# Performance work log

Measured on AMD Instinct MI355X. Metric: run time of the kernel, lower is better.

Reference implementation:

```python
import jax, jax.numpy as jnp
import numpy as np

B, S, D_MODEL, H_DIM = 8, 4096, 512, 120  # h = 1, so d_k = h_dim = 120
NEG_INF = jnp.float32(-1e9)
L2_EPS = 1e-12  # F.normalize eps


def setup_inputs() -> dict:
    key = jax.random.key(0)
    k_q, k_m, k_w, k_wt = jax.random.split(key, 4)
    query = jax.random.normal(k_q, (B, S, D_MODEL), dtype=jnp.float32)
    mask = jax.random.randint(k_m, (B, S, S), 0, 2, dtype=jnp.int32)
    # q_linear params (kaiming-uniform-ish init scale)
    lim = 1.0 / np.sqrt(D_MODEL)
    w_q = jax.random.uniform(k_w, (H_DIM, D_MODEL), jnp.float32, -lim, lim)
    b_q = jnp.zeros((H_DIM,), jnp.float32)
    # weight_tensor: shape (h, d_k) = (1, 120), xavier-uniform scale
    wt_lim = np.sqrt(6.0 / (1 + H_DIM))
    weight_tensor = jax.random.uniform(k_wt, (1, H_DIM), jnp.float32, -wt_lim, wt_lim)
    return {"query": query, "mask": mask, "w_q": w_q, "b_q": b_q,
            "weight_tensor": weight_tensor}


def reference(query, mask, w_q, b_q, weight_tensor):
    # context = q_linear(query).view(B, -1, h_dim); with h=1 the view is identity
    context = jnp.einsum("bsd,kd->bsk", query, w_q) + b_q          # [B, S, 120]
    # weighted then L2-normalized (cosine-similarity) features
    ctx = context * weight_tensor[:, None, :]                        # bcast (1,1,120)
    norm = jnp.sqrt(jnp.sum(ctx * ctx, axis=-1, keepdims=True))
    ctx_n = ctx / jnp.maximum(norm, L2_EPS)
    scores = jnp.einsum("bqk,bpk->bqp", ctx_n, ctx_n)               # [B, S, S]
    scores = jnp.where(mask == 0, NEG_INF, scores)                   # masked_fill
    return jax.nn.softmax(scores, axis=-1)                           # dropout: eval/identity
```

## Files before the change

kernel.cpp:

```cpp
#include <hip/hip_runtime.h>
#include <hip/hip_bf16.h>
#include <stdint.h>

#define BATCH 8
#define SEQ   4096
#define DM    512
#define HD    120
#define KP    128

typedef __bf16   v8bf  __attribute__((ext_vector_type(8)));
typedef float    v4f   __attribute__((ext_vector_type(4)));
typedef uint32_t u32x4 __attribute__((ext_vector_type(4)));
typedef uint32_t u32x2 __attribute__((ext_vector_type(2)));
typedef float    f32x4 __attribute__((ext_vector_type(4)));

static __device__ __forceinline__ ushort f2bf(float x) {
  uint32_t u = __builtin_bit_cast(uint32_t, x);
  return (ushort)((u + 0x7fffu + ((u >> 16) & 1u)) >> 16);
}

static __device__ __forceinline__ void gld16(const void* g, void* l) {
  __builtin_amdgcn_global_load_lds(
      (const __attribute__((address_space(1))) uint32_t*)g,
      (__attribute__((address_space(3))) uint32_t*)l, 16, 0, 0);
}

template <int NC>
static __device__ __forceinline__ void stage(const char* gsrc, char* lbase, int w, int lane) {
  #pragma unroll
  for (int i = 0; i < NC; ++i)
    gld16(gsrc + (w * NC + i) * 1024 + lane * 16, lbase + (w * NC + i) * 1024);
}

__global__ __launch_bounds__(256) void ctx_kernel(
    const float* __restrict__ q, const float* __restrict__ wq,
    const float* __restrict__ bq, const float* __restrict__ wt,
    ushort* __restrict__ ctx)
{
  __shared__ __align__(16) float qs[32][68];
  __shared__ __align__(16) float ws2[32][136];

  const int t  = threadIdx.x;
  const int tx = t & 31, ty = t >> 5;
  const size_t row0 = (size_t)blockIdx.x * 64;
  const int qr = t >> 2, qk = (t & 3) * 8;

  float acc[8][4];
  #pragma unroll
  for (int j = 0; j < 8; ++j)
    #pragma unroll
    for (int i = 0; i < 4; ++i) acc[j][i] = 0.f;

  for (int k0 = 0; k0 < DM; k0 += 32) {
    __syncthreads();
    {
      f32x4 v0 = *(const f32x4*)&q[(row0 + qr) * DM + k0 + qk];
      f32x4 v1 = *(const f32x4*)&q[(row0 + qr) * DM + k0 + qk + 4];
      #pragma unroll
      for (int i = 0; i < 4; ++i) qs[qk + i][qr] = v0[i];
      #pragma unroll
      for (int i = 0; i < 4; ++i) qs[qk + 4 + i][qr] = v1[i];
    }
    #pragma unroll
    for (int i = 0; i < 16; ++i) {
      int flat = t + i * 256;
      int kk = flat & 31, c = flat >> 5;
      ws2[kk][c] = (c < HD) ? wq[c * DM + k0 + kk] : 0.f;
    }
    __syncthreads();
    #pragma unroll
    for (int kk = 0; kk < 32; ++kk) {
      f32x4 b  = *(const f32x4*)&ws2[kk][tx * 4];
      f32x4 a0 = *(const f32x4*)&qs[kk][ty * 8];
      f32x4 a1 = *(const f32x4*)&qs[kk][ty * 8 + 4];
      #pragma unroll
      for (int r = 0; r < 4; ++r)
        #pragma unroll
        for (int c = 0; c < 4; ++c) {
          acc[r][c]     = fmaf(a0[r], b[c], acc[r][c]);
          acc[4 + r][c] = fmaf(a1[r], b[c], acc[4 + r][c]);
        }
    }
  }

  float wtv[4], bqv[4];
  #pragma unroll
  for (int i = 0; i < 4; ++i) {
    int c = tx * 4 + i;
    wtv[i] = (c < HD) ? wt[c] : 0.f;
    bqv[i] = (c < HD) ? bq[c] : 0.f;
  }
  #pragma unroll
  for (int j = 0; j < 8; ++j) {
    int r = ty * 8 + j;
    float v[4]; float ss = 0.f;
    #pragma unroll
    for (int i = 0; i < 4; ++i) {
      v[i] = (acc[j][i] + bqv[i]) * wtv[i];
      ss = fmaf(v[i], v[i], ss);
    }
    #pragma unroll
    for (int xm = 1; xm < 32; xm <<= 1) ss += __shfl_xor(ss, xm, 64);
    float rinv = 1.f / fmaxf(sqrtf(ss), 1e-12f);
    uint32_t p0 = (uint32_t)f2bf(v[0] * rinv) | ((uint32_t)f2bf(v[1] * rinv) << 16);
    uint32_t p1 = (uint32_t)f2bf(v[2] * rinv) | ((uint32_t)f2bf(v[3] * rinv) << 16);
    u32x2 o = {p0, p1};
    char* dst = (char*)ctx + (row0 + r) * 256 +
                (((tx >> 1) * 16) ^ ((r & 7) << 4)) + (tx & 1) * 8;
    *(u32x2*)dst = o;
  }
}

static __device__ __forceinline__ v8bf ldfrag(const char* base, int row, int kb) {
  int byte = row * 256 + (kb ^ ((row & 7) << 4));
  return __builtin_bit_cast(v8bf, *(const u32x4*)(base + byte));
}

#define DO_MFMA(BUF, ACC)                                                        \
  _Pragma("unroll")                                                              \
  for (int kk = 0; kk < 4; ++kk) {                                               \
    int kb = kk * 64 + g * 16;                                                   \
    v8bf a0 = ldfrag(A_s, wr * 32 + ln, kb);                                     \
    v8bf a1 = ldfrag(A_s, wr * 32 + 16 + ln, kb);                                \
    v8bf b0 = ldfrag(BUF, wc * 32 + ln, kb);                                     \
    v8bf b1 = ldfrag(BUF, wc * 32 + 16 + ln, kb);                                \
    ACC[0][0] = __builtin_amdgcn_mfma_f32_16x16x32_bf16(a0, b0, ACC[0][0], 0, 0, 0); \
    ACC[0][1] = __builtin_amdgcn_mfma_f32_16x16x32_bf16(a0, b1, ACC[0][1], 0, 0, 0); \
    ACC[1][0] = __builtin_amdgcn_mfma_f32_16x16x32_bf16(a1, b0, ACC[1][0], 0, 0, 0); \
    ACC[1][1] = __builtin_amdgcn_mfma_f32_16x16x32_bf16(a1, b1, ACC[1][1], 0, 0, 0); \
  }

#define LOADM(dst, jj)                                                           \
  do {                                                                           \
    int joff = (jj) * 128;                                                       \
    _Pragma("unroll") for (int rs = 0; rs < 2; ++rs)                             \
    _Pragma("unroll") for (int i2 = 0; i2 < 4; ++i2)                             \
    _Pragma("unroll") for (int cs = 0; cs < 2; ++cs)                             \
      dst[rs * 8 + cs * 4 + i2] = mrow[rs][i2][joff + cs * 16];                  \
  } while (0)

__global__ __launch_bounds__(512) void attn_kernel(
    const ushort* __restrict__ ctx, const int* __restrict__ mask,
    uint32_t* __restrict__ wsbits, float* __restrict__ out)
{
  __shared__ __align__(16) char lds[81920];
  char* A_s = lds;
  char* B0  = lds + 16384;
  char* B1  = lds + 49152;
  float* lW   = (float*)B1;
  float* lfin = (float*)(B1 + 1024);

  const int t    = threadIdx.x;
  const int b    = blockIdx.x & 7;
  const int tile = blockIdx.x >> 3;
  const int r0   = tile * 64;
  const int w    = t >> 6, lane = t & 63;
  const int wr   = w >> 2, wc = w & 3;
  const int g    = lane >> 4, ln = lane & 15;
  const char* ctxb = (const char*)ctx + (size_t)b * SEQ * 256;
  uint32_t* wsb = wsbits + (size_t)blockIdx.x * (512 * 16);
  const size_t mbase = ((size_t)b << 24) + ((size_t)r0 << 12);

  const int* mrow[2][4];
  #pragma unroll
  for (int rs = 0; rs < 2; ++rs)
    #pragma unroll
    for (int i = 0; i < 4; ++i) {
      int qrr = wr * 32 + rs * 16 + g * 4 + i;
      mrow[rs][i] = mask + mbase + ((size_t)qrr << 12) + wc * 32 + ln;
    }

  stage<2>(ctxb + (size_t)r0 * 256, A_s, w, lane);
  stage<4>(ctxb, B0, w, lane);
  int mcur[16];
  LOADM(mcur, 0);
  __syncthreads();

  float lpart[2][4];
  #pragma unroll
  for (int rs = 0; rs < 2; ++rs)
    #pragma unroll
    for (int i = 0; i < 4; ++i) lpart[rs][i] = 0.f;
  uint32_t curbits = 0;

  for (int j = 0; j < 32; ++j) {
    char* cur = (j & 1) ? B1 : B0;
    char* nxt = (j & 1) ? B0 : B1;
    if (j < 31) stage<4>(ctxb + (size_t)((j + 1) * 128) * 256, nxt, w, lane);
    int mnext[16];
    if (j < 31) LOADM(mnext, j + 1);

    v4f acc[2][2];
    #pragma unroll
    for (int rs = 0; rs < 2; ++rs)
      #pragma unroll
      for (int cs = 0; cs < 2; ++cs) acc[rs][cs] = (v4f){0.f, 0.f, 0.f, 0.f};
    DO_MFMA(cur, acc);

    uint32_t tb = 0;
    #pragma unroll
    for (int rs = 0; rs < 2; ++rs)
      #pragma unroll
      for (int cs = 0; cs < 2; ++cs)
        #pragma unroll
        for (int i = 0; i < 4; ++i) {
          int mk = mcur[rs * 8 + cs * 4 + i];
          float e = mk ? __expf(acc[rs][cs][i] - 1.0f) : 0.0f;
          lpart[rs][i] += e;
          tb |= (uint32_t)(mk != 0) << (rs * 8 + cs * 4 + i);
        }
    if (j & 1) wsb[(j >> 1) * 512 + t] = curbits | (tb << 16);
    else       curbits = tb;
    if (j < 31) {
      #pragma unroll
      for (int x = 0; x < 16; ++x) mcur[x] = mnext[x];
    }
    __syncthreads();
  }

  #pragma unroll
  for (int rs = 0; rs < 2; ++rs)
    #pragma unroll
    for (int i = 0; i < 4; ++i) {
      float s = lpart[rs][i];
      #pragma unroll
      for (int xm = 1; xm < 16; xm <<= 1) s += __shfl_xor(s, xm, 64);
      lpart[rs][i] = s;
    }
  if (ln == 0) {
    #pragma unroll
    for (int rs = 0; rs < 2; ++rs)
      #pragma unroll
      for (int i = 0; i < 4; ++i)
        lW[wc * 64 + wr * 32 + rs * 16 + g * 4 + i] = lpart[rs][i];
  }
  __syncthreads();
  if (t < 64) {
    float lf = lW[t] + lW[64 + t] + lW[128 + t] + lW[192 + t];
    lfin[t] = (lf > 0.f) ? (1.f / lf) : 0.f;
  }
  __syncthreads();
  float lir[2][4];
  #pragma unroll
  for (int rs = 0; rs < 2; ++rs)
    #pragma unroll
    for (int i = 0; i < 4; ++i)
      lir[rs][i] = lfin[wr * 32 + rs * 16 + g * 4 + i];

  stage<4>(ctxb, B0, w, lane);
  uint32_t bcur = wsb[t];
  uint32_t bnext = 0;
  __syncthreads();

  for (int j = 0; j < 32; ++j) {
    char* cur = (j & 1) ? B1 : B0;
    char* nxt = (j & 1) ? B0 : B1;
    if (j < 31) stage<4>(ctxb + (size_t)((j + 1) * 128) * 256, nxt, w, lane);
    if (!(j & 1) && j < 30) bnext = wsb[((j >> 1) + 1) * 512 + t];

    v4f acc[2][2];
    #pragma unroll
    for (int rs = 0; rs < 2; ++rs)
      #pragma unroll
      for (int cs = 0; cs < 2; ++cs) acc[rs][cs] = (v4f){0.f, 0.f, 0.f, 0.f};
    DO_MFMA(cur, acc);

    uint32_t bits = bcur >> ((j & 1) * 16);
    #pragma unroll
    for (int rs = 0; rs < 2; ++rs)
      #pragma unroll
      for (int cs = 0; cs < 2; ++cs)
        #pragma unroll
        for (int i = 0; i < 4; ++i) {
          int qrr = wr * 32 + rs * 16 + g * 4 + i;
          size_t off = mbase + ((size_t)qrr << 12) + j * 128 + wc * 32 + cs * 16 + ln;
          float val = ((bits >> (rs * 8 + cs * 4 + i)) & 1u)
                        ? __expf(acc[rs][cs][i] - 1.0f) * lir[rs][i] : 0.0f;
          __builtin_nontemporal_store(val, out + off);
        }
    if (j & 1) bcur = bnext;
    __syncthreads();
  }
}

extern "C" void kernel_launch(void* const* d_in, const int* in_sizes, int n_in,
                              void* d_out, int out_size, void* d_ws, size_t ws_size,
                              hipStream_t stream) {
  const float* query = (const float*)d_in[0];
  const int*   mask  = (const int*)d_in[1];
  const float* w_q   = (const float*)d_in[2];
  const float* b_q   = (const float*)d_in[3];
  const float* wt    = (const float*)d_in[4];
  float* out = (float*)d_out;

  ushort* ctx = (ushort*)d_ws;
  uint32_t* wsbits = (uint32_t*)((char*)d_ws +
      (size_t)BATCH * SEQ * KP * sizeof(ushort));

  ctx_kernel<<<dim3(BATCH * SEQ / 64), dim3(256), 0, stream>>>(query, w_q, b_q, wt, ctx);
  attn_kernel<<<dim3(BATCH * SEQ / 64), dim3(512), 0, stream>>>(ctx, mask, wsbits, out);
}
```

Before: 356.4 us.

## Restructure attention kernel to per-wave row strips with register-resident Q and direct global loads

Replaces the LDS-staged, block-tiled two-pass attention kernel with one where each wave owns 16 query rows, keeps its Q fragments in registers, and streams key fragments straight from global memory into registers with software double buffering. This removes LDS staging and the __syncthreads barriers. Mask and output accesses become 16-byte vector loads and stores along rows, and the ctx layout drops its XOR swizzle. The grid shrinks to 512 blocks of 256 threads, so occupancy falls, and key data is re-read from global or L2 by every wave instead of being shared through LDS.

```diff
diff --git a/kernel.cpp b/kernel.cpp
--- a/kernel.cpp
+++ b/kernel.cpp
@@ -6,30 +6,16 @@
 #define SEQ   4096
 #define DM    512
 #define HD    120
-#define KP    128
 
 typedef __bf16   v8bf  __attribute__((ext_vector_type(8)));
 typedef float    v4f   __attribute__((ext_vector_type(4)));
-typedef uint32_t u32x4 __attribute__((ext_vector_type(4)));
+typedef int      i4    __attribute__((ext_vector_type(4)));
 typedef uint32_t u32x2 __attribute__((ext_vector_type(2)));
 typedef float    f32x4 __attribute__((ext_vector_type(4)));
 
 static __device__ __forceinline__ ushort f2bf(float x) {
   uint32_t u = __builtin_bit_cast(uint32_t, x);
   return (ushort)((u + 0x7fffu + ((u >> 16) & 1u)) >> 16);
-}
-
-static __device__ __forceinline__ void gld16(const void* g, void* l) {
-  __builtin_amdgcn_global_load_lds(
-      (const __attribute__((address_space(1))) uint32_t*)g,
-      (__attribute__((address_space(3))) uint32_t*)l, 16, 0, 0);
-}
-
-template <int NC>
-static __device__ __forceinline__ void stage(const char* gsrc, char* lbase, int w, int lane) {
-  #pragma unroll
-  for (int i = 0; i < NC; ++i)
-    gld16(gsrc + (w * NC + i) * 1024 + lane * 16, lbase + (w * NC + i) * 1024);
 }
 
 __global__ __launch_bounds__(256) void ctx_kernel(
@@ -70,15 +56,15 @@
     __syncthreads();
     #pragma unroll
     for (int kk = 0; kk < 32; ++kk) {
-      f32x4 b  = *(const f32x4*)&ws2[kk][tx * 4];
+      f32x4 bv = *(const f32x4*)&ws2[kk][tx * 4];
       f32x4 a0 = *(const f32x4*)&qs[kk][ty * 8];
       f32x4 a1 = *(const f32x4*)&qs[kk][ty * 8 + 4];
       #pragma unroll
       for (int r = 0; r < 4; ++r)
         #pragma unroll
         for (int c = 0; c < 4; ++c) {
-          acc[r][c]     = fmaf(a0[r], b[c], acc[r][c]);
-          acc[4 + r][c] = fmaf(a1[r], b[c], acc[4 + r][c]);
+          acc[r][c]     = fmaf(a0[r], bv[c], acc[r][c]);
+          acc[4 + r][c] = fmaf(a1[r], bv[c], acc[4 + r][c]);
         }
     }
   }
@@ -105,181 +91,118 @@
     uint32_t p0 = (uint32_t)f2bf(v[0] * rinv) | ((uint32_t)f2bf(v[1] * rinv) << 16);
     uint32_t p1 = (uint32_t)f2bf(v[2] * rinv) | ((uint32_t)f2bf(v[3] * rinv) << 16);
     u32x2 o = {p0, p1};
-    char* dst = (char*)ctx + (row0 + r) * 256 +
-                (((tx >> 1) * 16) ^ ((r & 7) << 4)) + (tx & 1) * 8;
-    *(u32x2*)dst = o;
-  }
-}
-
-static __device__ __forceinline__ v8bf ldfrag(const char* base, int row, int kb) {
-  int byte = row * 256 + (kb ^ ((row & 7) << 4));
-  return __builtin_bit_cast(v8bf, *(const u32x4*)(base + byte));
-}
-
-#define DO_MFMA(BUF, ACC)                                                        \
-  _Pragma("unroll")                                                              \
-  for (int kk = 0; kk < 4; ++kk) {                                               \
-    int kb = kk * 64 + g * 16;                                                   \
-    v8bf a0 = ldfrag(A_s, wr * 32 + ln, kb);                                     \
-    v8bf a1 = ldfrag(A_s, wr * 32 + 16 + ln, kb);                                \
-    v8bf b0 = ldfrag(BUF, wc * 32 + ln, kb);                                     \
-    v8bf b1 = ldfrag(BUF, wc * 32 + 16 + ln, kb);                                \
-    ACC[0][0] = __builtin_amdgcn_mfma_f32_16x16x32_bf16(a0, b0, ACC[0][0], 0, 0, 0); \
-    ACC[0][1] = __builtin_amdgcn_mfma_f32_16x16x32_bf16(a0, b1, ACC[0][1], 0, 0, 0); \
-    ACC[1][0] = __builtin_amdgcn_mfma_f32_16x16x32_bf16(a1, b0, ACC[1][0], 0, 0, 0); \
-    ACC[1][1] = __builtin_amdgcn_mfma_f32_16x16x32_bf16(a1, b1, ACC[1][1], 0, 0, 0); \
-  }
-
-#define LOADM(dst, jj)                                                           \
-  do {                                                                           \
-    int joff = (jj) * 128;                                                       \
-    _Pragma("unroll") for (int rs = 0; rs < 2; ++rs)                             \
-    _Pragma("unroll") for (int i2 = 0; i2 < 4; ++i2)                             \
-    _Pragma("unroll") for (int cs = 0; cs < 2; ++cs)                             \
-      dst[rs * 8 + cs * 4 + i2] = mrow[rs][i2][joff + cs * 16];                  \
-  } while (0)
-
-__global__ __launch_bounds__(512) void attn_kernel(
+    *(u32x2*)((char*)ctx + (row0 + r) * 256 + tx * 8) = o;
+  }
+}
+
+#define MFMA(A, B, C) __builtin_amdgcn_mfma_f32_16x16x32_bf16(A, B, C, 0, 0, 0)
+
+#define LDP(dst, jc) do {                                                     \
+  const char* _p = ctxb + (size_t)((jc) * 32 + ln) * 256 + g * 16;            \
+  dst[0] = *(const v8bf*)(_p);         dst[1] = *(const v8bf*)(_p + 64);      \
+  dst[2] = *(const v8bf*)(_p + 128);   dst[3] = *(const v8bf*)(_p + 192);     \
+  dst[4] = *(const v8bf*)(_p + 4096);  dst[5] = *(const v8bf*)(_p + 4160);    \
+  dst[6] = *(const v8bf*)(_p + 4224);  dst[7] = *(const v8bf*)(_p + 4288);    \
+} while (0)
+
+#define LDM(dst, jc) do {                                                     \
+  dst[0] = *(const i4*)(mrow + (jc) * 32 + g * 4);                            \
+  dst[1] = *(const i4*)(mrow + (jc) * 32 + 16 + g * 4);                       \
+} while (0)
+
+#define QKT(pf, a0, a1) do {                                                  \
+  a0 = (v4f){0.f, 0.f, 0.f, 0.f}; a1 = (v4f){0.f, 0.f, 0.f, 0.f};             \
+  a0 = MFMA(pf[0], qf0, a0);  a1 = MFMA(pf[4], qf0, a1);                      \
+  a0 = MFMA(pf[1], qf1, a0);  a1 = MFMA(pf[5], qf1, a1);                      \
+  a0 = MFMA(pf[2], qf2, a0);  a1 = MFMA(pf[6], qf2, a1);                      \
+  a0 = MFMA(pf[3], qf3, a0);  a1 = MFMA(pf[7], qf3, a1);                      \
+} while (0)
+
+#define STEPA(pf, mf, jc, SH) do {                                            \
+  v4f a0, a1; QKT(pf, a0, a1);                                                \
+  uint32_t tb = 0;                                                            \
+  _Pragma("unroll")                                                           \
+  for (int i = 0; i < 4; ++i) {                                               \
+    float e0 = __expf(a0[i] - 1.f), e1 = __expf(a1[i] - 1.f);                 \
+    lsum += (mf[0][i] ? e0 : 0.f) + (mf[1][i] ? e1 : 0.f);                    \
+    tb |= (uint32_t)(mf[0][i] != 0) << i;                                     \
+    tb |= (uint32_t)(mf[1][i] != 0) << (4 + i);                               \
+  }                                                                           \
+  ubits |= tb << (SH);                                                        \
+  if ((SH) == 24) { wsb[((jc) >> 2) * 64 + lane] = ubits; ubits = 0; }        \
+} while (0)
+
+#define STEPB(pf, jc, SH) do {                                                \
+  v4f a0, a1; QKT(pf, a0, a1);                                                \
+  uint32_t bb = bcur >> (SH);                                                 \
+  f32x4 o0, o1;                                                               \
+  _Pragma("unroll")                                                           \
+  for (int i = 0; i < 4; ++i) {                                               \
+    o0[i] = ((bb >> i) & 1u)       ? __expf(a0[i] - 1.f) * lir : 0.f;         \
+    o1[i] = ((bb >> (4 + i)) & 1u) ? __expf(a1[i] - 1.f) * lir : 0.f;         \
+  }                                                                           \
+  *(f32x4*)(orow + (size_t)(jc) * 32 + g * 4) = o0;                           \
+  *(f32x4*)(orow + (size_t)(jc) * 32 + 16 + g * 4) = o1;                      \
+} while (0)
+
+__global__ __launch_bounds__(256) void attn_kernel(
     const ushort* __restrict__ ctx, const int* __restrict__ mask,
     uint32_t* __restrict__ wsbits, float* __restrict__ out)
 {
-  __shared__ __align__(16) char lds[81920];
-  char* A_s = lds;
-  char* B0  = lds + 16384;
-  char* B1  = lds + 49152;
-  float* lW   = (float*)B1;
-  float* lfin = (float*)(B1 + 1024);
-
   const int t    = threadIdx.x;
   const int b    = blockIdx.x & 7;
-  const int tile = blockIdx.x >> 3;
-  const int r0   = tile * 64;
   const int w    = t >> 6, lane = t & 63;
-  const int wr   = w >> 2, wc = w & 3;
-  const int g    = lane >> 4, ln = lane & 15;
+  const int ln   = lane & 15, g = lane >> 4;
+  const int qg   = (blockIdx.x >> 3) * 4 + w;
+  const int qrow = qg * 16 + ln;
   const char* ctxb = (const char*)ctx + (size_t)b * SEQ * 256;
-  uint32_t* wsb = wsbits + (size_t)blockIdx.x * (512 * 16);
-  const size_t mbase = ((size_t)b << 24) + ((size_t)r0 << 12);
-
-  const int* mrow[2][4];
-  #pragma unroll
-  for (int rs = 0; rs < 2; ++rs)
-    #pragma unroll
-    for (int i = 0; i < 4; ++i) {
-      int qrr = wr * 32 + rs * 16 + g * 4 + i;
-      mrow[rs][i] = mask + mbase + ((size_t)qrr << 12) + wc * 32 + ln;
-    }
-
-  stage<2>(ctxb + (size_t)r0 * 256, A_s, w, lane);
-  stage<4>(ctxb, B0, w, lane);
-  int mcur[16];
-  LOADM(mcur, 0);
-  __syncthreads();
-
-  float lpart[2][4];
-  #pragma unroll
-  for (int rs = 0; rs < 2; ++rs)
-    #pragma unroll
-    for (int i = 0; i < 4; ++i) lpart[rs][i] = 0.f;
-  uint32_t curbits = 0;
-
-  for (int j = 0; j < 32; ++j) {
-    char* cur = (j & 1) ? B1 : B0;
-    char* nxt = (j & 1) ? B0 : B1;
-    if (j < 31) stage<4>(ctxb + (size_t)((j + 1) * 128) * 256, nxt, w, lane);
-    int mnext[16];
-    if (j < 31) LOADM(mnext, j + 1);
-
-    v4f acc[2][2];
-    #pragma unroll
-    for (int rs = 0; rs < 2; ++rs)
-      #pragma unroll
-      for (int cs = 0; cs < 2; ++cs) acc[rs][cs] = (v4f){0.f, 0.f, 0.f, 0.f};
-    DO_MFMA(cur, acc);
-
-    uint32_t tb = 0;
-    #pragma unroll
-    for (int rs = 0; rs < 2; ++rs)
-      #pragma unroll
-      for (int cs = 0; cs < 2; ++cs)
-        #pragma unroll
-        for (int i = 0; i < 4; ++i) {
-          int mk = mcur[rs * 8 + cs * 4 + i];
-          float e = mk ? __expf(acc[rs][cs][i] - 1.0f) : 0.0f;
-          lpart[rs][i] += e;
-          tb |= (uint32_t)(mk != 0) << (rs * 8 + cs * 4 + i);
-        }
-    if (j & 1) wsb[(j >> 1) * 512 + t] = curbits | (tb << 16);
-    else       curbits = tb;
-    if (j < 31) {
-      #pragma unroll
-      for (int x = 0; x < 16; ++x) mcur[x] = mnext[x];
-    }
-    __syncthreads();
-  }
-
-  #pragma unroll
-  for (int rs = 0; rs < 2; ++rs)
-    #pragma unroll
-    for (int i = 0; i < 4; ++i) {
-      float s = lpart[rs][i];
-      #pragma unroll
-      for (int xm = 1; xm < 16; xm <<= 1) s += __shfl_xor(s, xm, 64);
-      lpart[rs][i] = s;
-    }
-  if (ln == 0) {
-    #pragma unroll
-    for (int rs = 0; rs < 2; ++rs)
-      #pragma unroll
-      for (int i = 0; i < 4; ++i)
-        lW[wc * 64 + wr * 32 + rs * 16 + g * 4 + i] = lpart[rs][i];
-  }
-  __syncthreads();
-  if (t < 64) {
-    float lf = lW[t] + lW[64 + t] + lW[128 + t] + lW[192 + t];
-    lfin[t] = (lf > 0.f) ? (1.f / lf) : 0.f;
-  }
-  __syncthreads();
-  float lir[2][4];
-  #pragma unroll
-  for (int rs = 0; rs < 2; ++rs)
-    #pragma unroll
-    for (int i = 0; i < 4; ++i)
-      lir[rs][i] = lfin[wr * 32 + rs * 16 + g * 4 + i];
-
-  stage<4>(ctxb, B0, w, lane);
-  uint32_t bcur = wsb[t];
-  uint32_t bnext = 0;
-  __syncthreads();
-
-  for (int j = 0; j < 32; ++j) {
-    char* cur = (j & 1) ? B1 : B0;
-    char* nxt = (j & 1) ? B0 : B1;
-    if (j < 31) stage<4>(ctxb + (size_t)((j + 1) * 128) * 256, nxt, w, lane);
-    if (!(j & 1) && j < 30) bnext = wsb[((j >> 1) + 1) * 512 + t];
-
-    v4f acc[2][2];
-    #pragma unroll
-    for (int rs = 0; rs < 2; ++rs)
-      #pragma unroll
-      for (int cs = 0; cs < 2; ++cs) acc[rs][cs] = (v4f){0.f, 0.f, 0.f, 0.f};
-    DO_MFMA(cur, acc);
-
-    uint32_t bits = bcur >> ((j & 1) * 16);
-    #pragma unroll
-    for (int rs = 0; rs < 2; ++rs)
-      #pragma unroll
-      for (int cs = 0; cs < 2; ++cs)
-        #pragma unroll
-        for (int i = 0; i < 4; ++i) {
-          int qrr = wr * 32 + rs * 16 + g * 4 + i;
-          size_t off = mbase + ((size_t)qrr << 12) + j * 128 + wc * 32 + cs * 16 + ln;
-          float val = ((bits >> (rs * 8 + cs * 4 + i)) & 1u)
-                        ? __expf(acc[rs][cs][i] - 1.0f) * lir[rs][i] : 0.0f;
-          __builtin_nontemporal_store(val, out + off);
-        }
-    if (j & 1) bcur = bnext;
-    __syncthreads();
+  const size_t obase = ((size_t)b * SEQ + qrow) * SEQ;
+  const int*  __restrict__ mrow = mask + obase;
+  float*      __restrict__ orow = out + obase;
+  uint32_t*   __restrict__ wsb  = wsbits + ((size_t)blockIdx.x * 4 + w) * 2048;
+
+  const char* qp = ctxb + (size_t)qrow * 256 + g * 16;
+  const v8bf qf0 = *(const v8bf*)(qp);
+  const v8bf qf1 = *(const v8bf*)(qp + 64);
+  const v8bf qf2 = *(const v8bf*)(qp + 128);
+  const v8bf qf3 = *(const v8bf*)(qp + 192);
+
+  v8bf pA[8], pB[8];
+  i4   mA[2], mB[2];
+  float lsum = 0.f;
+  uint32_t ubits = 0;
+
+  LDP(pA, 0); LDM(mA, 0);
+  for (int j4 = 0; j4 < 128; j4 += 4) {
+    LDP(pB, j4 + 1); LDM(mB, j4 + 1);
+    STEPA(pA, mA, j4, 0);
+    LDP(pA, j4 + 2); LDM(mA, j4 + 2);
+    STEPA(pB, mB, j4 + 1, 8);
+    LDP(pB, j4 + 3); LDM(mB, j4 + 3);
+    STEPA(pA, mA, j4 + 2, 16);
+    if (j4 + 4 < 128) { LDP(pA, j4 + 4); LDM(mA, j4 + 4); }
+    STEPA(pB, mB, j4 + 3, 24);
+  }
+
+  lsum += __shfl_xor(lsum, 16, 64);
+  lsum += __shfl_xor(lsum, 32, 64);
+  const float lir = (lsum > 0.f) ? (1.f / lsum) : 0.f;
+
+  asm volatile("s_waitcnt vmcnt(0)" ::: "memory");
+
+  uint32_t bcur = wsb[lane];
+  LDP(pA, 0);
+  for (int j4 = 0; j4 < 128; j4 += 4) {
+    uint32_t bnxt = (j4 + 4 < 128) ? wsb[((j4 >> 2) + 1) * 64 + lane] : 0u;
+    LDP(pB, j4 + 1);
+    STEPB(pA, j4, 0);
+    LDP(pA, j4 + 2);
+    STEPB(pB, j4 + 1, 8);
+    LDP(pB, j4 + 3);
+    STEPB(pA, j4 + 2, 16);
+    if (j4 + 4 < 128) LDP(pA, j4 + 4);
+    STEPB(pB, j4 + 3, 24);
+    bcur = bnxt;
   }
 }
 
@@ -293,10 +216,9 @@
   const float* wt    = (const float*)d_in[4];
   float* out = (float*)d_out;
 
-  ushort* ctx = (ushort*)d_ws;
-  uint32_t* wsbits = (uint32_t*)((char*)d_ws +
-      (size_t)BATCH * SEQ * KP * sizeof(ushort));
+  ushort*   ctx    = (ushort*)d_ws;
+  uint32_t* wsbits = (uint32_t*)((char*)d_ws + (16u << 20));
 
   ctx_kernel<<<dim3(BATCH * SEQ / 64), dim3(256), 0, stream>>>(query, w_q, b_q, wt, ctx);
-  attn_kernel<<<dim3(BATCH * SEQ / 64), dim3(512), 0, stream>>>(ctx, mask, wsbits, out);
-}
+  attn_kernel<<<dim3(512), dim3(256), 0, stream>>>(ctx, mask, wsbits, out);
+}
```

Result: slower. 681.0 us (+91.1%).
